# Kernel tuning notes

Hardware: AMD Instinct MI355X
Metric: run time of the kernel (lower is better)

Reference implementation:

```python
import jax, jax.numpy as jnp
import numpy as np

N_NODES = 50000
N_EDGES = 800000
IN_C, HID_C, OUT_C = 128, 128, 64


def setup_inputs() -> dict:
    key = jax.random.key(0)
    ks = jax.random.split(key, 8)
    x = jax.random.normal(ks[0], (N_NODES, IN_C), dtype=jnp.float32)
    edge_index = jax.random.randint(ks[1], (2, N_EDGES), 0, N_NODES, dtype=jnp.int64)
    def glorot(k, shape):
        lim = np.sqrt(6.0 / (shape[0] + shape[1])).astype(np.float32)
        return jax.random.uniform(k, shape, jnp.float32, -lim, lim)
    return {
        "x": x,
        "edge_index": edge_index,
        "W1l": glorot(ks[2], (IN_C, HID_C)),
        "b1": jnp.zeros((HID_C,), jnp.float32),
        "W1r": glorot(ks[3], (IN_C, HID_C)),
        "W2l": glorot(ks[4], (HID_C, OUT_C)),
        "b2": jnp.zeros((OUT_C,), jnp.float32),
        "W2r": glorot(ks[5], (HID_C, OUT_C)),
    }


def _sage_conv(h, src, dst, Wl, bl, Wr):
    # mean aggregation over incoming edges (source -> target)
    n = h.shape[0]
    msg_sum = jax.ops.segment_sum(h[src], dst, num_segments=n)          # [N, d]
    deg = jax.ops.segment_sum(jnp.ones((src.shape[0],), h.dtype), dst, num_segments=n)
    agg = msg_sum / jnp.maximum(deg, 1.0)[:, None]                      # zero-degree -> 0
    # lin_l(agg) + lin_r(h); lin_l carries the bias (PyG SAGEConv default)
    return agg @ Wl + bl + h @ Wr


def reference(x, edge_index, W1l, b1, W1r, W2l, b2, W2r):
    src, dst = edge_index[0], edge_index[1]
    h = jax.nn.relu(_sage_conv(x, src, dst, W1l, b1, W1r))
    # eval-mode forward: dropout is identity
    out = _sage_conv(h, src, dst, W2l, b2, W2r)
    return out
```

## Files before the change

kernel.cpp:

```cpp
#include <hip/hip_runtime.h>

#define N_NODES 50000
#define N_EDGES 800000
#define IN_C    128
#define HID_C   128
#define OUT_C   64
#define NQ      784
#define QBCAP   1536
#define QCAP    1536
#define EPB     2048
#define EBLKS   ((N_EDGES + EPB - 1) / EPB)
#define PACK_BLKS 192
#define MM1_BLKS  ((N_NODES + 63) / 64)
#define L2F_BLKS  NQ
#define HS_STRIDE 136

typedef unsigned short ushort_t;
typedef unsigned int   uint_t;
typedef unsigned char  uchar_t;
typedef __attribute__((ext_vector_type(8))) short bf16x8;
typedef __attribute__((ext_vector_type(4))) float f32x4;
typedef __attribute__((ext_vector_type(2))) float f32x2;

__device__ inline ushort_t f2bf(float f) {
    uint_t u = __float_as_uint(f);
    uint_t r = (u + 0x7fffu + ((u >> 16) & 1u)) >> 16;
    return (ushort_t)r;
}
__device__ inline float bflo(uint_t v) { return __uint_as_float(v << 16); }
__device__ inline float bfhi(uint_t v) { return __uint_as_float(v & 0xffff0000u); }
__device__ inline uchar_t f2fp8(float v) {
    return (uchar_t)(__builtin_amdgcn_cvt_pk_fp8_f32(v, v, 0, false) & 0xff);
}
__device__ inline void acc_fp8x4(float* a, uint_t d) {
    const f32x2 lo = __builtin_amdgcn_cvt_pk_f32_fp8((int)d, false);
    const f32x2 hi = __builtin_amdgcn_cvt_pk_f32_fp8((int)d, true);
    a[0] += lo.x; a[1] += lo.y; a[2] += hi.x; a[3] += hi.y;
}

__device__ inline void pack_one(const float* W, ushort_t* Wp, int K, int N, int idx) {
    const int j  = idx & 7;
    const int L  = (idx >> 3) & 63;
    const int t  = idx >> 9;
    const int KT = K / 32;
    const int kt = t % KT;
    const int ct = t / KT;
    const int k  = kt * 32 + (L >> 4) * 8 + j;
    const int n  = ct * 16 + (L & 15);
    Wp[idx] = f2bf(W[k * N + n]);
}

__global__ __launch_bounds__(256) void k0_kernel(
    const float* __restrict__ W1l, const float* __restrict__ W1r,
    const float* __restrict__ W2l, const float* __restrict__ W2r,
    ushort_t* __restrict__ wpack, int* __restrict__ gcur)
{
    const int b = blockIdx.x;
    if (b < PACK_BLKS) {
        const int tid = b * 256 + threadIdx.x;
        if (tid < 16384)      pack_one(W1l, wpack,          IN_C,  HID_C, tid);
        else if (tid < 32768) pack_one(W1r, wpack + 16384,  IN_C,  HID_C, tid - 16384);
        else if (tid < 40960) pack_one(W2l, wpack + 32768,  HID_C, OUT_C, tid - 32768);
        else if (tid < 49152) pack_one(W2r, wpack + 40960,  HID_C, OUT_C, tid - 40960);
    } else {
        for (int i = threadIdx.x; i < NQ; i += 256) gcur[i] = 0;
    }
}

__device__ inline void mm1_body(int bid, const float* __restrict__ x,
                                const ushort_t* __restrict__ wpack,
                                uchar_t* __restrict__ p1f, ushort_t* __restrict__ t1b)
{
    const int wave = threadIdx.x >> 6;
    const int lane = threadIdx.x & 63;
    const int quad = lane >> 4;
    const int m    = lane & 15;
    const int row0 = bid * 64 + wave * 16;
    const int arow = min(row0 + m, N_NODES - 1);

    const bf16x8* Bl = (const bf16x8*)(wpack);
    const bf16x8* Br = (const bf16x8*)(wpack + 16384);

    f32x4 accl[8], accr[8];
#pragma unroll
    for (int ct = 0; ct < 8; ++ct) { accl[ct] = (f32x4)(0.0f); accr[ct] = (f32x4)(0.0f); }

#pragma unroll
    for (int kt = 0; kt < 4; ++kt) {
        const float* xp = x + (size_t)arow * IN_C + kt * 32 + quad * 8;
        const float4 a0 = *(const float4*)(xp);
        const float4 a1 = *(const float4*)(xp + 4);
        bf16x8 af;
        af[0] = (short)f2bf(a0.x); af[1] = (short)f2bf(a0.y);
        af[2] = (short)f2bf(a0.z); af[3] = (short)f2bf(a0.w);
        af[4] = (short)f2bf(a1.x); af[5] = (short)f2bf(a1.y);
        af[6] = (short)f2bf(a1.z); af[7] = (short)f2bf(a1.w);
#pragma unroll
        for (int ct = 0; ct < 8; ++ct) {
            const bf16x8 bl = Bl[(ct * 4 + kt) * 64 + lane];
            const bf16x8 br = Br[(ct * 4 + kt) * 64 + lane];
            accl[ct] = __builtin_amdgcn_mfma_f32_16x16x32_bf16(af, bl, accl[ct], 0, 0, 0);
            accr[ct] = __builtin_amdgcn_mfma_f32_16x16x32_bf16(af, br, accr[ct], 0, 0, 0);
        }
    }

#pragma unroll
    for (int r = 0; r < 4; ++r) {
        const int orow = row0 + quad * 4 + r;
        if (orow < N_NODES) {
#pragma unroll
            for (int ct = 0; ct < 8; ++ct) {
                const int col = ct * 16 + m;
                p1f[(size_t)orow * HID_C + col] = f2fp8(accl[ct][r]);
                t1b[(size_t)orow * HID_C + col] = f2bf(accr[ct][r]);
            }
        }
    }
}

__global__ __launch_bounds__(256) void k1_kernel(
    const float* __restrict__ x, const ushort_t* __restrict__ wpack,
    uchar_t* __restrict__ p1f, ushort_t* __restrict__ t1b,
    const int* __restrict__ src, const int* __restrict__ dst,
    int* gcur, int* __restrict__ ebuf)
{
    __shared__ int lh[NQ], gb2[NQ], lc[NQ];
    const int b = blockIdx.x;
    if (b < MM1_BLKS) {
        mm1_body(b, x, wpack, p1f, t1b);
        return;
    }
    const int blk = b - MM1_BLKS;
    const int t = threadIdx.x;
    for (int i = t; i < NQ; i += 256) lh[i] = 0;
    __syncthreads();
    const int e0 = blk * EPB + t * 8;
    int v8[8], b8[8];
    if (e0 < N_EDGES) {
        const int4 sa = *(const int4*)&src[e0];
        const int4 sb = *(const int4*)&src[e0 + 4];
        const int4 da = *(const int4*)&dst[e0];
        const int4 db = *(const int4*)&dst[e0 + 4];
        const int s8a[8] = {sa.x, sa.y, sa.z, sa.w, sb.x, sb.y, sb.z, sb.w};
        const int d8a[8] = {da.x, da.y, da.z, da.w, db.x, db.y, db.z, db.w};
#pragma unroll
        for (int j = 0; j < 8; ++j) {
            b8[j] = d8a[j] >> 6;
            v8[j] = (s8a[j] << 6) | (d8a[j] & 63);
            atomicAdd(&lh[b8[j]], 1);
        }
    } else {
#pragma unroll
        for (int j = 0; j < 8; ++j) b8[j] = -1;
    }
    __syncthreads();
    for (int i = t; i < NQ; i += 256) {
        const int run = lh[i];
        gb2[i] = (run > 0) ? atomicAdd(&gcur[i], run) : 0;
        lc[i] = 0;
    }
    __syncthreads();
#pragma unroll
    for (int j = 0; j < 8; ++j) {
        const int bk = b8[j];
        if (bk >= 0) {
            const int p   = atomicAdd(&lc[bk], 1);
            const int pos = gb2[bk] + p;
            if (pos < QBCAP) ebuf[bk * QBCAP + pos] = v8[j];
        }
    }
}

__global__ __launch_bounds__(256, 4) void l2f_kernel(
    const int* __restrict__ ebuf, const int* __restrict__ gcur,
    int* __restrict__ cnt, int* __restrict__ row_ptr, int* __restrict__ csr_g,
    const uchar_t* __restrict__ p1f, const ushort_t* __restrict__ t1b,
    const float* __restrict__ b1,
    const ushort_t* __restrict__ wpack,
    uchar_t* __restrict__ p2f, ushort_t* __restrict__ t2b)
{
    __shared__ ushort_t hs[64 * HS_STRIDE];
    __shared__ int csr_lds[QCAP];
    __shared__ int lh[64], lstart[64], lcur2[64];
    __shared__ int pool;

    const int blk = blockIdx.x;
    const int tid = threadIdx.x;

    if (tid == 0) pool = 0;
    if (tid < 64) lh[tid] = 0;
    __syncthreads();

    const int nb   = min(gcur[blk], QBCAP);
    const int base = blk * QBCAP;
    int v0 = -1, v1 = -1, v2 = -1, v3 = -1, v4 = -1, v5 = -1;
    if (tid        < nb) v0 = ebuf[base + tid];
    if (tid + 256  < nb) v1 = ebuf[base + tid + 256];
    if (tid + 512  < nb) v2 = ebuf[base + tid + 512];
    if (tid + 768  < nb) v3 = ebuf[base + tid + 768];
    if (tid + 1024 < nb) v4 = ebuf[base + tid + 1024];
    if (tid + 1280 < nb) v5 = ebuf[base + tid + 1280];
    if (v0 >= 0) atomicAdd(&lh[v0 & 63], 1);
    if (v1 >= 0) atomicAdd(&lh[v1 & 63], 1);
    if (v2 >= 0) atomicAdd(&lh[v2 & 63], 1);
    if (v3 >= 0) atomicAdd(&lh[v3 & 63], 1);
    if (v4 >= 0) atomicAdd(&lh[v4 & 63], 1);
    if (v5 >= 0) atomicAdd(&lh[v5 & 63], 1);
    __syncthreads();
    int scanv = 0;
    if (tid < 64) scanv = lh[tid];
    if (tid < 64) lcur2[tid] = scanv;
    __syncthreads();
#pragma unroll
    for (int off = 1; off < 64; off <<= 1) {
        int add = 0;
        if (tid < 64 && tid >= off) add = lcur2[tid - off];
        __syncthreads();
        if (tid < 64) lcur2[tid] += add;
        __syncthreads();
    }
    if (tid < 64) {
        const int ex = lcur2[tid] - scanv;
        lstart[tid] = ex;
        const int node = blk * 64 + tid;
        if (node < N_NODES) { cnt[node] = scanv; row_ptr[node] = blk * QCAP + ex; }
    }
    __syncthreads();
    if (tid < 64) lcur2[tid] = lstart[tid];
    __syncthreads();
    if (v0 >= 0) { const int p = atomicAdd(&lcur2[v0 & 63], 1); if (p < QCAP) csr_lds[p] = v0 >> 6; }
    if (v1 >= 0) { const int p = atomicAdd(&lcur2[v1 & 63], 1); if (p < QCAP) csr_lds[p] = v1 >> 6; }
    if (v2 >= 0) { const int p = atomicAdd(&lcur2[v2 & 63], 1); if (p < QCAP) csr_lds[p] = v2 >> 6; }
    if (v3 >= 0) { const int p = atomicAdd(&lcur2[v3 & 63], 1); if (p < QCAP) csr_lds[p] = v3 >> 6; }
    if (v4 >= 0) { const int p = atomicAdd(&lcur2[v4 & 63], 1); if (p < QCAP) csr_lds[p] = v4 >> 6; }
    if (v5 >= 0) { const int p = atomicAdd(&lcur2[v5 & 63], 1); if (p < QCAP) csr_lds[p] = v5 >> 6; }
    __syncthreads();
    {
        const int total = lcur2[63] > QCAP ? QCAP : lcur2[63];
        for (int i = tid; i < total; i += 256) csr_g[blk * QCAP + i] = csr_lds[i];
    }
    __syncthreads();

    const int c16 = tid & 7;
    const int gb  = (tid & 63) & 56;
    const uint4* p1v = (const uint4*)p1f;

    while (true) {
        int nl = 0;
        if (c16 == 0) nl = atomicAdd(&pool, 1);
        nl = __shfl(nl, gb, 64);
        if (nl >= 64) break;
        const int node = blk * 64 + nl;
        uint4 oL = make_uint4(0u, 0u, 0u, 0u);
        uint4 oH = make_uint4(0u, 0u, 0u, 0u);
        if (node < N_NODES) {
            const int start = lstart[nl];
            const int degi  = lh[nl];
            const size_t ib = (size_t)node * HID_C + c16 * 16;
            const uint4 tvL = *(const uint4*)(t1b + ib);
            const uint4 tvH = *(const uint4*)(t1b + ib + 8);
            float a[16];
#pragma unroll
            for (int z = 0; z < 16; ++z) a[z] = 0.0f;
            int e = 0;
            for (; e + 3 < degi; e += 4) {
                const int s0 = csr_lds[start + e];
                const int s1 = csr_lds[start + e + 1];
                const int s2 = csr_lds[start + e + 2];
                const int s3 = csr_lds[start + e + 3];
                const uint4 w0 = p1v[(size_t)s0 * 8 + c16];
                const uint4 w1 = p1v[(size_t)s1 * 8 + c16];
                const uint4 w2 = p1v[(size_t)s2 * 8 + c16];
                const uint4 w3 = p1v[(size_t)s3 * 8 + c16];
#pragma unroll
                for (int qq = 0; qq < 4; ++qq) {
                    const uint4 v = (qq == 0) ? w0 : (qq == 1) ? w1 : (qq == 2) ? w2 : w3;
                    acc_fp8x4(a + 0,  v.x);
                    acc_fp8x4(a + 4,  v.y);
                    acc_fp8x4(a + 8,  v.z);
                    acc_fp8x4(a + 12, v.w);
                }
            }
            for (; e < degi; ++e) {
                const uint4 v = p1v[(size_t)csr_lds[start + e] * 8 + c16];
                acc_fp8x4(a + 0,  v.x);
                acc_fp8x4(a + 4,  v.y);
                acc_fp8x4(a + 8,  v.z);
                acc_fp8x4(a + 12, v.w);
            }
            const float inv = 1.0f / fmaxf((float)degi, 1.0f);
            float r[16];
#pragma unroll
            for (int z = 0; z < 4; ++z) {
                const float4 bv = *(const float4*)(b1 + c16 * 16 + z * 4);
                r[z*4+0] = bv.x; r[z*4+1] = bv.y; r[z*4+2] = bv.z; r[z*4+3] = bv.w;
            }
            const uint_t tw[8] = {tvL.x, tvL.y, tvL.z, tvL.w, tvH.x, tvH.y, tvH.z, tvH.w};
#pragma unroll
            for (int z = 0; z < 8; ++z) {
                r[z*2+0] = fmaxf(fmaf(a[z*2+0], inv, r[z*2+0] + bflo(tw[z])), 0.0f);
                r[z*2+1] = fmaxf(fmaf(a[z*2+1], inv, r[z*2+1] + bfhi(tw[z])), 0.0f);
            }
            oL.x = (uint_t)f2bf(r[0])  | ((uint_t)f2bf(r[1])  << 16);
            oL.y = (uint_t)f2bf(r[2])  | ((uint_t)f2bf(r[3])  << 16);
            oL.z = (uint_t)f2bf(r[4])  | ((uint_t)f2bf(r[5])  << 16);
            oL.w = (uint_t)f2bf(r[6])  | ((uint_t)f2bf(r[7])  << 16);
            oH.x = (uint_t)f2bf(r[8])  | ((uint_t)f2bf(r[9])  << 16);
            oH.y = (uint_t)f2bf(r[10]) | ((uint_t)f2bf(r[11]) << 16);
            oH.z = (uint_t)f2bf(r[12]) | ((uint_t)f2bf(r[13]) << 16);
            oH.w = (uint_t)f2bf(r[14]) | ((uint_t)f2bf(r[15]) << 16);
        }
        *(uint4*)&hs[nl * HS_STRIDE + c16 * 16] = oL;
        *(uint4*)&hs[nl * HS_STRIDE + c16 * 16 + 8] = oH;
    }
    __syncthreads();

    const int wv   = tid >> 6;
    const int lane = tid & 63;
    const int quad = lane >> 4;
    const int m    = lane & 15;
    const int row0 = blk * 64 + wv * 16;

    const bf16x8* Bl = (const bf16x8*)(wpack + 32768);
    const bf16x8* Br = (const bf16x8*)(wpack + 40960);

    f32x4 accl[4], accr[4];
#pragma unroll
    for (int ct = 0; ct < 4; ++ct) { accl[ct] = (f32x4)(0.0f); accr[ct] = (f32x4)(0.0f); }

#pragma unroll
    for (int kt = 0; kt < 4; ++kt) {
        const bf16x8 af = *(const bf16x8*)&hs[(wv * 16 + m) * HS_STRIDE + kt * 32 + quad * 8];
#pragma unroll
        for (int ct = 0; ct < 4; ++ct) {
            const bf16x8 bl = Bl[(ct * 4 + kt) * 64 + lane];
            const bf16x8 br = Br[(ct * 4 + kt) * 64 + lane];
            accl[ct] = __builtin_amdgcn_mfma_f32_16x16x32_bf16(af, bl, accl[ct], 0, 0, 0);
            accr[ct] = __builtin_amdgcn_mfma_f32_16x16x32_bf16(af, br, accr[ct], 0, 0, 0);
        }
    }

#pragma unroll
    for (int r = 0; r < 4; ++r) {
        const int orow = row0 + quad * 4 + r;
        if (orow < N_NODES) {
#pragma unroll
            for (int ct = 0; ct < 4; ++ct) {
                const int col = ct * 16 + m;
                p2f[(size_t)orow * OUT_C + col] = f2fp8(accl[ct][r]);
                t2b[(size_t)orow * OUT_C + col] = f2bf(accr[ct][r]);
            }
        }
    }
}

__global__ __launch_bounds__(256) void agg2_kernel(
    const uchar_t* __restrict__ p2f, const ushort_t* __restrict__ t2b,
    const float* __restrict__ b2, const int* __restrict__ row_ptr,
    const int* __restrict__ cnt, const int* __restrict__ csr,
    float* __restrict__ out)
{
    const int c16 = threadIdx.x & 3;
    const int grp = threadIdx.x >> 2;
    const uint4* p2v = (const uint4*)p2f;

    const int node = blockIdx.x * 64 + grp;
    if (node >= N_NODES) return;
    const int start = row_ptr[node];
    const int degi  = cnt[node];
    const size_t i = (size_t)node * OUT_C + c16 * 16;
    const uint4 tvL = *(const uint4*)(t2b + i);
    const uint4 tvH = *(const uint4*)(t2b + i + 8);
    float a[16];
#pragma unroll
    for (int z = 0; z < 16; ++z) a[z] = 0.0f;
    int e = 0;
    for (; e + 3 < degi; e += 4) {
        const int s0 = csr[start + e];
        const int s1 = csr[start + e + 1];
        const int s2 = csr[start + e + 2];
        const int s3 = csr[start + e + 3];
        const uint4 w0 = p2v[(size_t)s0 * 4 + c16];
        const uint4 w1 = p2v[(size_t)s1 * 4 + c16];
        const uint4 w2 = p2v[(size_t)s2 * 4 + c16];
        const uint4 w3 = p2v[(size_t)s3 * 4 + c16];
#pragma unroll
        for (int q = 0; q < 4; ++q) {
            const uint4 v = (q == 0) ? w0 : (q == 1) ? w1 : (q == 2) ? w2 : w3;
            acc_fp8x4(a + 0,  v.x);
            acc_fp8x4(a + 4,  v.y);
            acc_fp8x4(a + 8,  v.z);
            acc_fp8x4(a + 12, v.w);
        }
    }
    for (; e < degi; ++e) {
        const uint4 v = p2v[(size_t)csr[start + e] * 4 + c16];
        acc_fp8x4(a + 0,  v.x);
        acc_fp8x4(a + 4,  v.y);
        acc_fp8x4(a + 8,  v.z);
        acc_fp8x4(a + 12, v.w);
    }

    const float inv = 1.0f / fmaxf((float)degi, 1.0f);
    const uint_t tw[8] = {tvL.x, tvL.y, tvL.z, tvL.w, tvH.x, tvH.y, tvH.z, tvH.w};
#pragma unroll
    for (int z = 0; z < 4; ++z) {
        const float4 bv = *(const float4*)(b2 + c16 * 16 + z * 4);
        float4 o;
        o.x = fmaf(a[z*4+0], inv, bv.x + bflo(tw[z*2+0]));
        o.y = fmaf(a[z*4+1], inv, bv.y + bfhi(tw[z*2+0]));
        o.z = fmaf(a[z*4+2], inv, bv.z + bflo(tw[z*2+1]));
        o.w = fmaf(a[z*4+3], inv, bv.w + bfhi(tw[z*2+1]));
        *(float4*)(out + i + z * 4) = o;
    }
}

extern "C" void kernel_launch(void* const* d_in, const int* in_sizes, int n_in,
                              void* d_out, int out_size, void* d_ws, size_t ws_size,
                              hipStream_t stream)
{
    const float* x   = (const float*)d_in[0];
    const int*   ei  = (const int*)d_in[1];
    const float* W1l = (const float*)d_in[2];
    const float* b1  = (const float*)d_in[3];
    const float* W1r = (const float*)d_in[4];
    const float* W2l = (const float*)d_in[5];
    const float* b2  = (const float*)d_in[6];
    const float* W2r = (const float*)d_in[7];
    float* out = (float*)d_out;

    const int* src = ei;
    const int* dst = ei + N_EDGES;

    const size_t NH = (size_t)N_NODES * HID_C;
    const size_t NO = (size_t)N_NODES * OUT_C;
    const size_t EB = (size_t)NQ * QBCAP;
    const size_t CB = (size_t)NQ * QCAP;

    char* ws = (char*)d_ws;
    ushort_t* t1b   = (ushort_t*)ws;                   ws += NH * sizeof(ushort_t);
    ushort_t* t2b   = (ushort_t*)ws;                   ws += NO * sizeof(ushort_t);
    ushort_t* wpack = (ushort_t*)ws;                   ws += 49152 * sizeof(ushort_t);
    int* ebuf    = (int*)ws;                           ws += EB * sizeof(int);
    int* csr     = (int*)ws;                           ws += CB * sizeof(int);
    int* cnt     = (int*)ws;                           ws += N_NODES * sizeof(int);
    int* row_ptr = (int*)ws;                           ws += N_NODES * sizeof(int);
    int* gcur    = (int*)ws;                           ws += NQ * sizeof(int);
    ws += (16 - ((size_t)(ws - (char*)d_ws) & 15)) & 15;
    uchar_t* p1f = (uchar_t*)ws;                       ws += NH * sizeof(uchar_t);
    uchar_t* p2f = (uchar_t*)ws;                       ws += NO * sizeof(uchar_t);

    const size_t need = (size_t)(ws - (char*)d_ws);
    if (ws_size < need) return;

    k0_kernel<<<PACK_BLKS + 1, 256, 0, stream>>>(W1l, W1r, W2l, W2r, wpack, gcur);
    k1_kernel<<<MM1_BLKS + EBLKS, 256, 0, stream>>>(
        x, wpack, p1f, t1b, src, dst, gcur, ebuf);
    l2f_kernel<<<L2F_BLKS, 256, 0, stream>>>(
        ebuf, gcur, cnt, row_ptr, csr, p1f, t1b, b1, wpack, p2f, t2b);
    agg2_kernel<<<MM1_BLKS, 256, 0, stream>>>(
        p2f, t2b, b2, row_ptr, cnt, csr, out);
}
```

Baseline: 155.3 us.

## Unroll gathers by eight, prefetch x tiles, use shuffle scan and vector CSR copy

Adds an 8-way unrolled gather loop in both aggregation kernels so more independent neighbour-row loads are in flight per thread. The first matmul now loads the next k-slice of x before the MFMAs of the current one. In l2f the 64-entry prefix scan uses wavefront shuffles in place of a barrier-heavy LDS scan, and the CSR copy to global memory uses int4 stores. The cost is higher register pressure, and the vector copy can write up to three entries past the valid total within each block's slot.

Result: slower. 175.2 us (+12.8%).

```diff
diff --git a/kernel.cpp b/kernel.cpp
--- a/kernel.cpp
+++ b/kernel.cpp
@@ -37,6 +37,12 @@
     const f32x2 hi = __builtin_amdgcn_cvt_pk_f32_fp8((int)d, true);
     a[0] += lo.x; a[1] += lo.y; a[2] += hi.x; a[3] += hi.y;
 }
+__device__ inline void acc_uint4(float* a, const uint4 v) {
+    acc_fp8x4(a + 0,  v.x);
+    acc_fp8x4(a + 4,  v.y);
+    acc_fp8x4(a + 8,  v.z);
+    acc_fp8x4(a + 12, v.w);
+}
 
 __device__ inline void pack_one(const float* W, ushort_t* Wp, int K, int N, int idx) {
     const int j  = idx & 7;
@@ -85,16 +91,22 @@
 #pragma unroll
     for (int ct = 0; ct < 8; ++ct) { accl[ct] = (f32x4)(0.0f); accr[ct] = (f32x4)(0.0f); }
 
+    const float* xbase = x + (size_t)arow * IN_C + quad * 8;
+    float4 c0 = *(const float4*)(xbase);
+    float4 c1 = *(const float4*)(xbase + 4);
+
 #pragma unroll
     for (int kt = 0; kt < 4; ++kt) {
-        const float* xp = x + (size_t)arow * IN_C + kt * 32 + quad * 8;
-        const float4 a0 = *(const float4*)(xp);
-        const float4 a1 = *(const float4*)(xp + 4);
+        float4 n0 = c0, n1 = c1;
+        if (kt < 3) {
+            n0 = *(const float4*)(xbase + (kt + 1) * 32);
+            n1 = *(const float4*)(xbase + (kt + 1) * 32 + 4);
+        }
         bf16x8 af;
-        af[0] = (short)f2bf(a0.x); af[1] = (short)f2bf(a0.y);
-        af[2] = (short)f2bf(a0.z); af[3] = (short)f2bf(a0.w);
-        af[4] = (short)f2bf(a1.x); af[5] = (short)f2bf(a1.y);
-        af[6] = (short)f2bf(a1.z); af[7] = (short)f2bf(a1.w);
+        af[0] = (short)f2bf(c0.x); af[1] = (short)f2bf(c0.y);
+        af[2] = (short)f2bf(c0.z); af[3] = (short)f2bf(c0.w);
+        af[4] = (short)f2bf(c1.x); af[5] = (short)f2bf(c1.y);
+        af[6] = (short)f2bf(c1.z); af[7] = (short)f2bf(c1.w);
 #pragma unroll
         for (int ct = 0; ct < 8; ++ct) {
             const bf16x8 bl = Bl[(ct * 4 + kt) * 64 + lane];
@@ -102,6 +114,7 @@
             accl[ct] = __builtin_amdgcn_mfma_f32_16x16x32_bf16(af, bl, accl[ct], 0, 0, 0);
             accr[ct] = __builtin_amdgcn_mfma_f32_16x16x32_bf16(af, br, accr[ct], 0, 0, 0);
         }
+        c0 = n0; c1 = n1;
     }
 
 #pragma unroll
@@ -180,9 +193,9 @@
     uchar_t* __restrict__ p2f, ushort_t* __restrict__ t2b)
 {
     __shared__ ushort_t hs[64 * HS_STRIDE];
-    __shared__ int csr_lds[QCAP];
+    __shared__ __align__(16) int csr_lds[QCAP];
     __shared__ int lh[64], lstart[64], lcur2[64];
-    __shared__ int pool;
+    __shared__ int pool, ltotal;
 
     const int blk = blockIdx.x;
     const int tid = threadIdx.x;
@@ -207,26 +220,21 @@
     if (v4 >= 0) atomicAdd(&lh[v4 & 63], 1);
     if (v5 >= 0) atomicAdd(&lh[v5 & 63], 1);
     __syncthreads();
-    int scanv = 0;
-    if (tid < 64) scanv = lh[tid];
-    if (tid < 64) lcur2[tid] = scanv;
-    __syncthreads();
-#pragma unroll
-    for (int off = 1; off < 64; off <<= 1) {
-        int add = 0;
-        if (tid < 64 && tid >= off) add = lcur2[tid - off];
-        __syncthreads();
-        if (tid < 64) lcur2[tid] += add;
-        __syncthreads();
-    }
     if (tid < 64) {
-        const int ex = lcur2[tid] - scanv;
+        const int c = lh[tid];
+        int v = c;
+#pragma unroll
+        for (int off = 1; off < 64; off <<= 1) {
+            const int u = __shfl_up(v, off, 64);
+            if (tid >= off) v += u;
+        }
+        const int ex = v - c;
         lstart[tid] = ex;
+        lcur2[tid]  = ex;
+        if (tid == 63) ltotal = v;
         const int node = blk * 64 + tid;
-        if (node < N_NODES) { cnt[node] = scanv; row_ptr[node] = blk * QCAP + ex; }
-    }
-    __syncthreads();
-    if (tid < 64) lcur2[tid] = lstart[tid];
+        if (node < N_NODES) { cnt[node] = c; row_ptr[node] = blk * QCAP + ex; }
+    }
     __syncthreads();
     if (v0 >= 0) { const int p = atomicAdd(&lcur2[v0 & 63], 1); if (p < QCAP) csr_lds[p] = v0 >> 6; }
     if (v1 >= 0) { const int p = atomicAdd(&lcur2[v1 & 63], 1); if (p < QCAP) csr_lds[p] = v1 >> 6; }
@@ -236,8 +244,11 @@
     if (v5 >= 0) { const int p = atomicAdd(&lcur2[v5 & 63], 1); if (p < QCAP) csr_lds[p] = v5 >> 6; }
     __syncthreads();
     {
-        const int total = lcur2[63] > QCAP ? QCAP : lcur2[63];
-        for (int i = tid; i < total; i += 256) csr_g[blk * QCAP + i] = csr_lds[i];
+        const int total = ltotal > QCAP ? QCAP : ltotal;
+        const int nt4 = (total + 3) >> 2;
+        int4* dst4 = (int4*)(csr_g + blk * QCAP);
+        const int4* src4 = (const int4*)csr_lds;
+        for (int i = tid; i < nt4; i += 256) dst4[i] = src4[i];
     }
     __syncthreads();
 
@@ -263,8 +274,28 @@
 #pragma unroll
             for (int z = 0; z < 16; ++z) a[z] = 0.0f;
             int e = 0;
+            for (; e + 7 < degi; e += 8) {
+                const int s0 = csr_lds[start + e + 0];
+                const int s1 = csr_lds[start + e + 1];
+                const int s2 = csr_lds[start + e + 2];
+                const int s3 = csr_lds[start + e + 3];
+                const int s4 = csr_lds[start + e + 4];
+                const int s5 = csr_lds[start + e + 5];
+                const int s6 = csr_lds[start + e + 6];
+                const int s7 = csr_lds[start + e + 7];
+                const uint4 w0 = p1v[(size_t)s0 * 8 + c16];
+                const uint4 w1 = p1v[(size_t)s1 * 8 + c16];
+                const uint4 w2 = p1v[(size_t)s2 * 8 + c16];
+                const uint4 w3 = p1v[(size_t)s3 * 8 + c16];
+                const uint4 w4 = p1v[(size_t)s4 * 8 + c16];
+                const uint4 w5 = p1v[(size_t)s5 * 8 + c16];
+                const uint4 w6 = p1v[(size_t)s6 * 8 + c16];
+                const uint4 w7 = p1v[(size_t)s7 * 8 + c16];
+                acc_uint4(a, w0); acc_uint4(a, w1); acc_uint4(a, w2); acc_uint4(a, w3);
+                acc_uint4(a, w4); acc_uint4(a, w5); acc_uint4(a, w6); acc_uint4(a, w7);
+            }
             for (; e + 3 < degi; e += 4) {
-                const int s0 = csr_lds[start + e];
+                const int s0 = csr_lds[start + e + 0];
                 const int s1 = csr_lds[start + e + 1];
                 const int s2 = csr_lds[start + e + 2];
                 const int s3 = csr_lds[start + e + 3];
@@ -272,21 +303,11 @@
                 const uint4 w1 = p1v[(size_t)s1 * 8 + c16];
                 const uint4 w2 = p1v[(size_t)s2 * 8 + c16];
                 const uint4 w3 = p1v[(size_t)s3 * 8 + c16];
-#pragma unroll
-                for (int qq = 0; qq < 4; ++qq) {
-                    const uint4 v = (qq == 0) ? w0 : (qq == 1) ? w1 : (qq == 2) ? w2 : w3;
-                    acc_fp8x4(a + 0,  v.x);
-                    acc_fp8x4(a + 4,  v.y);
-                    acc_fp8x4(a + 8,  v.z);
-                    acc_fp8x4(a + 12, v.w);
-                }
+                acc_uint4(a, w0); acc_uint4(a, w1); acc_uint4(a, w2); acc_uint4(a, w3);
             }
             for (; e < degi; ++e) {
                 const uint4 v = p1v[(size_t)csr_lds[start + e] * 8 + c16];
-                acc_fp8x4(a + 0,  v.x);
-                acc_fp8x4(a + 4,  v.y);
-                acc_fp8x4(a + 8,  v.z);
-                acc_fp8x4(a + 12, v.w);
+                acc_uint4(a, v);
             }
             const float inv = 1.0f / fmaxf((float)degi, 1.0f);
             float r[16];
@@ -375,8 +396,28 @@
 #pragma unroll
     for (int z = 0; z < 16; ++z) a[z] = 0.0f;
     int e = 0;
+    for (; e + 7 < degi; e += 8) {
+        const int s0 = csr[start + e + 0];
+        const int s1 = csr[start + e + 1];
+        const int s2 = csr[start + e + 2];
+        const int s3 = csr[start + e + 3];
+        const int s4 = csr[start + e + 4];
+        const int s5 = csr[start + e + 5];
+        const int s6 = csr[start + e + 6];
+        const int s7 = csr[start + e + 7];
+        const uint4 w0 = p2v[(size_t)s0 * 4 + c16];
+        const uint4 w1 = p2v[(size_t)s1 * 4 + c16];
+        const uint4 w2 = p2v[(size_t)s2 * 4 + c16];
+        const uint4 w3 = p2v[(size_t)s3 * 4 + c16];
+        const uint4 w4 = p2v[(size_t)s4 * 4 + c16];
+        const uint4 w5 = p2v[(size_t)s5 * 4 + c16];
+        const uint4 w6 = p2v[(size_t)s6 * 4 + c16];
+        const uint4 w7 = p2v[(size_t)s7 * 4 + c16];
+        acc_uint4(a, w0); acc_uint4(a, w1); acc_uint4(a, w2); acc_uint4(a, w3);
+        acc_uint4(a, w4); acc_uint4(a, w5); acc_uint4(a, w6); acc_uint4(a, w7);
+    }
     for (; e + 3 < degi; e += 4) {
-        const int s0 = csr[start + e];
+        const int s0 = csr[start + e + 0];
         const int s1 = csr[start + e + 1];
         const int s2 = csr[start + e + 2];
         const int s3 = csr[start + e + 3];
@@ -384,21 +425,11 @@
         const uint4 w1 = p2v[(size_t)s1 * 4 + c16];
         const uint4 w2 = p2v[(size_t)s2 * 4 + c16];
         const uint4 w3 = p2v[(size_t)s3 * 4 + c16];
-#pragma unroll
-        for (int q = 0; q < 4; ++q) {
-            const uint4 v = (q == 0) ? w0 : (q == 1) ? w1 : (q == 2) ? w2 : w3;
-            acc_fp8x4(a + 0,  v.x);
-            acc_fp8x4(a + 4,  v.y);
-            acc_fp8x4(a + 8,  v.z);
-            acc_fp8x4(a + 12, v.w);
-        }
+        acc_uint4(a, w0); acc_uint4(a, w1); acc_uint4(a, w2); acc_uint4(a, w3);
     }
     for (; e < degi; ++e) {
         const uint4 v = p2v[(size_t)csr[start + e] * 4 + c16];
-        acc_fp8x4(a + 0,  v.x);
-        acc_fp8x4(a + 4,  v.y);
-        acc_fp8x4(a + 8,  v.z);
-        acc_fp8x4(a + 12, v.w);
+        acc_uint4(a, v);
     }
 
     const float inv = 1.0f / fmaxf((float)degi, 1.0f);
```
